# Optimization experiments

Measured on AMD Instinct MI355X. Metric: run time of the kernel, lower is better.

## Reference

```python
import jax, jax.numpy as jnp
import numpy as np

N = 100000
DEG = 16
E = N * DEG
IN_DIM = 256
HID = 64
OUT = 64


def setup_inputs() -> dict:
    key = jax.random.key(0)
    ks = jax.random.split(key, 6)
    x = jax.random.normal(ks[0], (N, IN_DIM), dtype=jnp.float32)
    # CSR with fixed degree DEG: row i owns edges [i*DEG, (i+1)*DEG)
    row_id = jnp.repeat(jnp.arange(N, dtype=jnp.int64), DEG)
    col_id = jax.random.randint(ks[1], (E,), 0, N, dtype=jnp.int64)
    adj = jnp.stack([col_id, row_id])  # adj[0]=col, adj[1]=row (matches torch forward)
    row_ptr = (jnp.arange(N + 1, dtype=jnp.int64) * DEG)
    W1 = jax.random.normal(ks[2], (IN_DIM, HID), dtype=jnp.float32) / np.sqrt(IN_DIM)
    b1 = jnp.zeros((HID,), dtype=jnp.float32)
    W2 = jax.random.normal(ks[3], (HID, OUT), dtype=jnp.float32) / np.sqrt(HID)
    b2 = jnp.zeros((OUT,), dtype=jnp.float32)
    return {"x": x, "adj": adj, "row_ptr": row_ptr, "W1": W1, "b1": b1, "W2": W2, "b2": b2}


def agnn_layer(x, row, col, beta):
    # x: [N, d]; row/col: [E]. AGNN: e_ij = beta*cos(x_i, x_j), row-softmax, aggregate x_j.
    norm = jnp.maximum(jnp.linalg.norm(x, axis=-1, keepdims=True), 1e-12)
    xn = x / norm  # [N, d]
    e = beta * jnp.sum(xn[row] * xn[col], axis=-1)  # [E] cosine scores
    # numerically stable segment softmax over rows
    m = jax.ops.segment_max(e, row, num_segments=N)  # [N]
    ex = jnp.exp(e - m[row])  # [E]
    denom = jax.ops.segment_sum(ex, row, num_segments=N)  # [N]
    alpha = ex / jnp.maximum(denom[row], 1e-12)  # [E]
    out = jax.ops.segment_sum(alpha[:, None] * x[col], row, num_segments=N)  # [N, d]
    return out


def reference(x, adj, row_ptr, W1, b1, W2, b2):
    col, row = adj[0], adj[1]
    beta = jnp.float32(1.0)  # non-trainable buffer, initialized to ones
    h = jax.nn.relu(x @ W1 + b1)
    for _ in range(4):
        h = jax.nn.relu(agnn_layer(h, row, col, beta))
    return h @ W2 + b2
```

## Files before the change

kernel.cpp:

```cpp
#include <hip/hip_runtime.h>
#include <math.h>

#define N_NODES 100000
#define DEG 16
#define IN_DIM 256
#define HID 64

typedef _Float16 f16x8 __attribute__((ext_vector_type(8)));
typedef _Float16 f16x4 __attribute__((ext_vector_type(4)));
typedef __fp16 fp16x2b __attribute__((ext_vector_type(2)));
typedef float f32x4 __attribute__((ext_vector_type(4)));

union F16x8u {
  f16x8 v;
  fp16x2b h2[4];
};

__global__ __launch_bounds__(256) void extract_col_kernel(const int* __restrict__ adj,
                                                          int* __restrict__ col, int E) {
  const bool is64 = (adj[2 * E - 1] == 0);
  for (int e = blockIdx.x * blockDim.x + threadIdx.x; e < E; e += gridDim.x * blockDim.x) {
    col[e] = is64 ? adj[2 * e] : adj[e];
  }
}

__global__ __launch_bounds__(256) void prep_wfrag_kernel(const float* __restrict__ W,
                                                         _Float16* __restrict__ wfrag,
                                                         int nfrag) {
  const int id = blockIdx.x * 256 + threadIdx.x;
  if (id >= nfrag) return;
  const int lane = id & 63;
  const int nt = (id >> 6) & 3;
  const int kt = id >> 8;
  const int k0 = kt * 32 + (lane >> 4) * 8;
  const int c = nt * 16 + (lane & 15);
  f16x8 v;
#pragma unroll
  for (int j = 0; j < 8; ++j) v[j] = (_Float16)W[(k0 + j) * HID + c];
  ((f16x8*)wfrag)[id] = v;
}

__global__ __launch_bounds__(256) void mlp1_kernel(const float* __restrict__ x,
                                                   const _Float16* __restrict__ wfrag,
                                                   const float* __restrict__ b1,
                                                   _Float16* __restrict__ hn,
                                                   float* __restrict__ nrm) {
  __shared__ f16x8 Bs[2048];
#pragma unroll
  for (int i = 0; i < 8; ++i)
    Bs[threadIdx.x + 256 * i] = ((const f16x8*)wfrag)[threadIdx.x + 256 * i];

  const int lane = threadIdx.x & 63;
  const int wv = threadIdx.x >> 6;
  const int rbase = blockIdx.x * 64 + wv * 16;
  const int arow = min(rbase + (lane & 15), N_NODES - 1);
  const int kgrp = lane >> 4;
  const float* xrow = x + (size_t)arow * IN_DIM + kgrp * 8;

  f32x4 acc[4];
#pragma unroll
  for (int nt = 0; nt < 4; ++nt) acc[nt] = {0.0f, 0.0f, 0.0f, 0.0f};

  __syncthreads();

#pragma unroll
  for (int kt = 0; kt < 8; ++kt) {
    const float4 a0 = *(const float4*)&xrow[kt * 32];
    const float4 a1 = *(const float4*)&xrow[kt * 32 + 4];
    F16x8u u;
    u.h2[0] = __builtin_amdgcn_cvt_pkrtz(a0.x, a0.y);
    u.h2[1] = __builtin_amdgcn_cvt_pkrtz(a0.z, a0.w);
    u.h2[2] = __builtin_amdgcn_cvt_pkrtz(a1.x, a1.y);
    u.h2[3] = __builtin_amdgcn_cvt_pkrtz(a1.z, a1.w);
#pragma unroll
    for (int nt = 0; nt < 4; ++nt)
      acc[nt] = __builtin_amdgcn_mfma_f32_16x16x32_f16(u.v, Bs[(kt * 4 + nt) * 64 + lane],
                                                       acc[nt], 0, 0, 0);
  }

  const int colb = lane & 15;
  float bias[4];
#pragma unroll
  for (int nt = 0; nt < 4; ++nt) bias[nt] = b1[nt * 16 + colb];

#pragma unroll
  for (int j = 0; j < 4; ++j) {
    float o[4];
#pragma unroll
    for (int nt = 0; nt < 4; ++nt) o[nt] = fmaxf(acc[nt][j] + bias[nt], 0.0f);
    float ss = o[0] * o[0] + o[1] * o[1] + o[2] * o[2] + o[3] * o[3];
    ss += __shfl_xor(ss, 1); ss += __shfl_xor(ss, 2);
    ss += __shfl_xor(ss, 4); ss += __shfl_xor(ss, 8);
    const float nv = sqrtf(ss);
    const float inv = 1.0f / fmaxf(nv, 1e-12f);
    const int row = rbase + kgrp * 4 + j;
    if (row < N_NODES) {
#pragma unroll
      for (int nt = 0; nt < 4; ++nt)
        hn[(size_t)row * HID + nt * 16 + colb] = (_Float16)(o[nt] * inv);
      if (colb == 0) nrm[row] = nv;
    }
  }
}

__global__ __launch_bounds__(256) void agnn_kernel(const _Float16* __restrict__ hn,
                                                   const float* __restrict__ nrm,
                                                   const int* __restrict__ col,
                                                   _Float16* __restrict__ hn_out,
                                                   float* __restrict__ nrm_out) {
  const int lane = threadIdx.x & 63;
  const int wv = threadIdx.x >> 6;
  const int g = lane >> 4;
  const int gl = lane & 15;
  const int node = blockIdx.x * 16 + wv * 4 + g;

  const f16x4* hp4 = (const f16x4*)hn;
  const f16x4 xiv = hp4[(size_t)node * 16 + gl];

  const int cidx = col[node * DEG + gl];
  const float ncv = nrm[cidx];

  const int vbase = (lane & 48) * 4;

  f16x4 xcv[DEG];
#pragma unroll
  for (int e = 0; e < DEG; ++e) {
    const int ce = __builtin_amdgcn_ds_bpermute(vbase + e * 4, cidx);
    xcv[e] = hp4[(size_t)((uint)ce * 16u + (uint)gl)];
  }

  const float x0 = (float)xiv[0], x1 = (float)xiv[1];
  const float x2 = (float)xiv[2], x3 = (float)xiv[3];
  float t[DEG];
#pragma unroll
  for (int e = 0; e < DEG; ++e) {
    float a = fmaf(x1, (float)xcv[e][1], x0 * (float)xcv[e][0]);
    float b = fmaf(x3, (float)xcv[e][3], x2 * (float)xcv[e][2]);
    t[e] = a + b;
  }

  const bool b0 = (lane & 1), b1 = (lane & 2), b2 = (lane & 4), b3 = (lane & 8);
  float u[8];
#pragma unroll
  for (int j = 0; j < 8; ++j) {
    const float keep = b0 ? t[2 * j + 1] : t[2 * j];
    const float send = b0 ? t[2 * j] : t[2 * j + 1];
    u[j] = keep + __shfl_xor(send, 1);
  }
  float v[4];
#pragma unroll
  for (int j = 0; j < 4; ++j) {
    const float keep = b1 ? u[2 * j + 1] : u[2 * j];
    const float send = b1 ? u[2 * j] : u[2 * j + 1];
    v[j] = keep + __shfl_xor(send, 2);
  }
  float w2[2];
#pragma unroll
  for (int j = 0; j < 2; ++j) {
    const float keep = b2 ? v[2 * j + 1] : v[2 * j];
    const float send = b2 ? v[2 * j] : v[2 * j + 1];
    w2[j] = keep + __shfl_xor(send, 4);
  }
  float p;
  {
    const float keep = b3 ? w2[1] : w2[0];
    const float send = b3 ? w2[0] : w2[1];
    p = keep + __shfl_xor(send, 8);
  }

  float m = p;
  m = fmaxf(m, __shfl_xor(m, 1)); m = fmaxf(m, __shfl_xor(m, 2));
  m = fmaxf(m, __shfl_xor(m, 4)); m = fmaxf(m, __shfl_xor(m, 8));
  const float ex = __expf(p - m);
  float dn = ex;
  dn += __shfl_xor(dn, 1); dn += __shfl_xor(dn, 2);
  dn += __shfl_xor(dn, 4); dn += __shfl_xor(dn, 8);
  const float wgt = (ex / dn) * ncv;

  float o0 = 0.0f, o1 = 0.0f, o2 = 0.0f, o3 = 0.0f;
#pragma unroll
  for (int e = 0; e < DEG; ++e) {
    const float we = __int_as_float(
        __builtin_amdgcn_ds_bpermute(vbase + e * 4, __float_as_int(wgt)));
    o0 = fmaf(we, (float)xcv[e][0], o0);
    o1 = fmaf(we, (float)xcv[e][1], o1);
    o2 = fmaf(we, (float)xcv[e][2], o2);
    o3 = fmaf(we, (float)xcv[e][3], o3);
  }
  o0 = fmaxf(o0, 0.0f); o1 = fmaxf(o1, 0.0f);
  o2 = fmaxf(o2, 0.0f); o3 = fmaxf(o3, 0.0f);

  float ss = fmaf(o0, o0, o1 * o1) + fmaf(o2, o2, o3 * o3);
  ss += __shfl_xor(ss, 1); ss += __shfl_xor(ss, 2);
  ss += __shfl_xor(ss, 4); ss += __shfl_xor(ss, 8);
  const float nv = sqrtf(ss);
  const float inv = 1.0f / fmaxf(nv, 1e-12f);

  f16x4 ov;
  ov[0] = (_Float16)(o0 * inv); ov[1] = (_Float16)(o1 * inv);
  ov[2] = (_Float16)(o2 * inv); ov[3] = (_Float16)(o3 * inv);
  ((f16x4*)hn_out)[(size_t)node * 16 + gl] = ov;
  if (gl == 0) nrm_out[node] = nv;
}

__global__ __launch_bounds__(256) void mlp2_kernel(const _Float16* __restrict__ hn,
                                                   const float* __restrict__ nrm,
                                                   const _Float16* __restrict__ w2frag,
                                                   const float* __restrict__ b2,
                                                   float* __restrict__ out) {
  __shared__ f16x8 Bs[512];
  if (threadIdx.x < 256) {
    Bs[threadIdx.x] = ((const f16x8*)w2frag)[threadIdx.x];
    Bs[threadIdx.x + 256] = ((const f16x8*)w2frag)[threadIdx.x + 256];
  }

  const int lane = threadIdx.x & 63;
  const int wv = threadIdx.x >> 6;
  const int rbase = blockIdx.x * 64 + wv * 16;
  const int arow = min(rbase + (lane & 15), N_NODES - 1);
  const int kgrp = lane >> 4;
  const _Float16* hrow = hn + (size_t)arow * HID + kgrp * 8;

  f32x4 acc[4];
#pragma unroll
  for (int nt = 0; nt < 4; ++nt) acc[nt] = {0.0f, 0.0f, 0.0f, 0.0f};

  __syncthreads();

#pragma unroll
  for (int kt = 0; kt < 2; ++kt) {
    const f16x8 a = *(const f16x8*)&hrow[kt * 32];
#pragma unroll
    for (int nt = 0; nt < 4; ++nt)
      acc[nt] = __builtin_amdgcn_mfma_f32_16x16x32_f16(a, Bs[(kt * 4 + nt) * 64 + lane],
                                                       acc[nt], 0, 0, 0);
  }

  const int colb = lane & 15;
  float bias[4];
#pragma unroll
  for (int nt = 0; nt < 4; ++nt) bias[nt] = b2[nt * 16 + colb];

#pragma unroll
  for (int j = 0; j < 4; ++j) {
    const int row = rbase + kgrp * 4 + j;
    const float rnv = nrm[min(row, N_NODES - 1)];
    if (row < N_NODES) {
#pragma unroll
      for (int nt = 0; nt < 4; ++nt)
        out[(size_t)row * HID + nt * 16 + colb] = fmaf(acc[nt][j], rnv, bias[nt]);
    }
  }
}

extern "C" void kernel_launch(void* const* d_in, const int* in_sizes, int n_in,
                              void* d_out, int out_size, void* d_ws, size_t ws_size,
                              hipStream_t stream) {
  const float* x = (const float*)d_in[0];
  const int* adj = (const int*)d_in[1];
  const float* W1 = (const float*)d_in[3];
  const float* b1 = (const float*)d_in[4];
  const float* W2 = (const float*)d_in[5];
  const float* b2 = (const float*)d_in[6];
  float* out = (float*)d_out;

  const int E = N_NODES * DEG;

  char* ws = (char*)d_ws;
  int* col = (int*)ws;
  ws += (size_t)E * sizeof(int);
  _Float16* wfrag = (_Float16*)ws;
  ws += (size_t)IN_DIM * HID * sizeof(_Float16);
  _Float16* w2frag = (_Float16*)ws;
  ws += (size_t)HID * HID * sizeof(_Float16);
  _Float16* hnA = (_Float16*)ws;
  ws += (size_t)N_NODES * HID * sizeof(_Float16);
  _Float16* hnB = (_Float16*)ws;
  ws += (size_t)N_NODES * HID * sizeof(_Float16);
  float* nrA = (float*)ws;
  ws += (size_t)N_NODES * sizeof(float);
  float* nrB = (float*)ws;

  hipLaunchKernelGGL(extract_col_kernel, dim3(2048), dim3(256), 0, stream, adj, col, E);
  hipLaunchKernelGGL(prep_wfrag_kernel, dim3(8), dim3(256), 0, stream, W1, wfrag, 2048);
  hipLaunchKernelGGL(prep_wfrag_kernel, dim3(2), dim3(256), 0, stream, W2, w2frag, 512);

  const int mlp_blocks = (N_NODES + 63) / 64;
  hipLaunchKernelGGL(mlp1_kernel, dim3(mlp_blocks), dim3(256), 0, stream, x, wfrag, b1, hnA, nrA);

  const int agnn_blocks = N_NODES / 16;
  hipLaunchKernelGGL(agnn_kernel, dim3(agnn_blocks), dim3(256), 0, stream, hnA, nrA, col, hnB, nrB);
  hipLaunchKernelGGL(agnn_kernel, dim3(agnn_blocks), dim3(256), 0, stream, hnB, nrB, col, hnA, nrA);
  hipLaunchKernelGGL(agnn_kernel, dim3(agnn_blocks), dim3(256), 0, stream, hnA, nrA, col, hnB, nrB);
  hipLaunchKernelGGL(agnn_kernel, dim3(agnn_blocks), dim3(256), 0, stream, hnB, nrB, col, hnA, nrA);

  hipLaunchKernelGGL(mlp2_kernel, dim3(mlp_blocks), dim3(256), 0, stream, hnA, nrA, w2frag, b2, out);
}
```

Measured before the change: 161.5 us.

## Remap AGNN kernel to 8 lanes per node with 16-byte gathers and fdot2

Each node now uses 8 lanes instead of 16, and each lane loads 8 fp16 features per neighbour (16-byte vector loads). The 16 edges are processed in two chunks of 8. Scores use packed fp16 dot-product instructions, and the softmax max-subtraction is dropped, relying on cosine scores being bounded by beta. The aim is fewer memory and ALU instructions per gathered row and fewer shuffle stages, at the cost of more registers per lane and half as many nodes' worth of blocks.

```diff
diff --git a/kernel.cpp b/kernel.cpp
--- a/kernel.cpp
+++ b/kernel.cpp
@@ -7,7 +7,6 @@
 #define HID 64
 
 typedef _Float16 f16x8 __attribute__((ext_vector_type(8)));
-typedef _Float16 f16x4 __attribute__((ext_vector_type(4)));
 typedef __fp16 fp16x2b __attribute__((ext_vector_type(2)));
 typedef float f32x4 __attribute__((ext_vector_type(4)));
 
@@ -15,6 +14,16 @@
   f16x8 v;
   fp16x2b h2[4];
 };
+
+#if __has_builtin(__builtin_amdgcn_fdot2)
+__device__ __forceinline__ float fdot2(fp16x2b a, fp16x2b b, float c) {
+  return __builtin_amdgcn_fdot2(a, b, c, false);
+}
+#else
+__device__ __forceinline__ float fdot2(fp16x2b a, fp16x2b b, float c) {
+  return fmaf((float)a[0], (float)b[0], fmaf((float)a[1], (float)b[1], c));
+}
+#endif
 
 __global__ __launch_bounds__(256) void extract_col_kernel(const int* __restrict__ adj,
                                                           int* __restrict__ col, int E) {
@@ -110,97 +119,107 @@
                                                    float* __restrict__ nrm_out) {
   const int lane = threadIdx.x & 63;
   const int wv = threadIdx.x >> 6;
-  const int g = lane >> 4;
-  const int gl = lane & 15;
-  const int node = blockIdx.x * 16 + wv * 4 + g;
-
-  const f16x4* hp4 = (const f16x4*)hn;
-  const f16x4 xiv = hp4[(size_t)node * 16 + gl];
-
-  const int cidx = col[node * DEG + gl];
-  const float ncv = nrm[cidx];
-
-  const int vbase = (lane & 48) * 4;
-
-  f16x4 xcv[DEG];
-#pragma unroll
-  for (int e = 0; e < DEG; ++e) {
-    const int ce = __builtin_amdgcn_ds_bpermute(vbase + e * 4, cidx);
-    xcv[e] = hp4[(size_t)((uint)ce * 16u + (uint)gl)];
-  }
-
-  const float x0 = (float)xiv[0], x1 = (float)xiv[1];
-  const float x2 = (float)xiv[2], x3 = (float)xiv[3];
-  float t[DEG];
-#pragma unroll
-  for (int e = 0; e < DEG; ++e) {
-    float a = fmaf(x1, (float)xcv[e][1], x0 * (float)xcv[e][0]);
-    float b = fmaf(x3, (float)xcv[e][3], x2 * (float)xcv[e][2]);
-    t[e] = a + b;
-  }
-
-  const bool b0 = (lane & 1), b1 = (lane & 2), b2 = (lane & 4), b3 = (lane & 8);
-  float u[8];
-#pragma unroll
-  for (int j = 0; j < 8; ++j) {
-    const float keep = b0 ? t[2 * j + 1] : t[2 * j];
-    const float send = b0 ? t[2 * j] : t[2 * j + 1];
-    u[j] = keep + __shfl_xor(send, 1);
-  }
-  float v[4];
-#pragma unroll
-  for (int j = 0; j < 4; ++j) {
-    const float keep = b1 ? u[2 * j + 1] : u[2 * j];
-    const float send = b1 ? u[2 * j] : u[2 * j + 1];
-    v[j] = keep + __shfl_xor(send, 2);
-  }
-  float w2[2];
-#pragma unroll
-  for (int j = 0; j < 2; ++j) {
-    const float keep = b2 ? v[2 * j + 1] : v[2 * j];
-    const float send = b2 ? v[2 * j] : v[2 * j + 1];
-    w2[j] = keep + __shfl_xor(send, 4);
-  }
-  float p;
-  {
-    const float keep = b3 ? w2[1] : w2[0];
-    const float send = b3 ? w2[0] : w2[1];
-    p = keep + __shfl_xor(send, 8);
-  }
-
-  float m = p;
-  m = fmaxf(m, __shfl_xor(m, 1)); m = fmaxf(m, __shfl_xor(m, 2));
-  m = fmaxf(m, __shfl_xor(m, 4)); m = fmaxf(m, __shfl_xor(m, 8));
-  const float ex = __expf(p - m);
-  float dn = ex;
-  dn += __shfl_xor(dn, 1); dn += __shfl_xor(dn, 2);
-  dn += __shfl_xor(dn, 4); dn += __shfl_xor(dn, 8);
-  const float wgt = (ex / dn) * ncv;
-
-  float o0 = 0.0f, o1 = 0.0f, o2 = 0.0f, o3 = 0.0f;
-#pragma unroll
-  for (int e = 0; e < DEG; ++e) {
-    const float we = __int_as_float(
-        __builtin_amdgcn_ds_bpermute(vbase + e * 4, __float_as_int(wgt)));
-    o0 = fmaf(we, (float)xcv[e][0], o0);
-    o1 = fmaf(we, (float)xcv[e][1], o1);
-    o2 = fmaf(we, (float)xcv[e][2], o2);
-    o3 = fmaf(we, (float)xcv[e][3], o3);
-  }
-  o0 = fmaxf(o0, 0.0f); o1 = fmaxf(o1, 0.0f);
-  o2 = fmaxf(o2, 0.0f); o3 = fmaxf(o3, 0.0f);
-
-  float ss = fmaf(o0, o0, o1 * o1) + fmaf(o2, o2, o3 * o3);
-  ss += __shfl_xor(ss, 1); ss += __shfl_xor(ss, 2);
-  ss += __shfl_xor(ss, 4); ss += __shfl_xor(ss, 8);
+  const int g = lane >> 3;
+  const int q = lane & 7;
+  const int node = blockIdx.x * 32 + wv * 8 + g;
+
+  const f16x8* hp8 = (const f16x8*)hn;
+  F16x8u xi;
+  xi.v = hp8[(size_t)node * 8 + q];
+
+  const int cidx0 = col[node * DEG + q];
+  const int cidx1 = col[node * DEG + 8 + q];
+  const float ncv0 = nrm[cidx0];
+  const float ncv1 = nrm[cidx1];
+
+  const int base = (lane & 56) * 4;
+
+  float o[8];
+#pragma unroll
+  for (int d = 0; d < 8; ++d) o[d] = 0.0f;
+  float dn = 0.0f;
+
+#pragma unroll
+  for (int c = 0; c < 2; ++c) {
+    const int cs = c ? cidx1 : cidx0;
+    const float ncv = c ? ncv1 : ncv0;
+
+    F16x8u xcv[8];
+#pragma unroll
+    for (int k = 0; k < 8; ++k) {
+      const int ce = __builtin_amdgcn_ds_bpermute(base + k * 4, cs);
+      xcv[k].v = hp8[(size_t)((uint)ce) * 8u + (uint)q];
+    }
+
+    float t[8];
+#pragma unroll
+    for (int k = 0; k < 8; ++k) {
+      float s = 0.0f;
+#pragma unroll
+      for (int j = 0; j < 4; ++j) s = fdot2(xi.h2[j], xcv[k].h2[j], s);
+      t[k] = s;
+    }
+
+    const bool b0 = (lane & 1), b1 = (lane & 2), b2 = (lane & 4);
+    float u[4];
+#pragma unroll
+    for (int j = 0; j < 4; ++j) {
+      const float keep = b0 ? t[2 * j + 1] : t[2 * j];
+      const float send = b0 ? t[2 * j] : t[2 * j + 1];
+      u[j] = keep + __shfl_xor(send, 1);
+    }
+    float v[2];
+#pragma unroll
+    for (int j = 0; j < 2; ++j) {
+      const float keep = b1 ? u[2 * j + 1] : u[2 * j];
+      const float send = b1 ? u[2 * j] : u[2 * j + 1];
+      v[j] = keep + __shfl_xor(send, 2);
+    }
+    float p;
+    {
+      const float keep = b2 ? v[1] : v[0];
+      const float send = b2 ? v[0] : v[1];
+      p = keep + __shfl_xor(send, 4);
+    }
+
+    const float ex = __expf(p);
+    dn += ex;
+    const float wgt = ex * ncv;
+
+#pragma unroll
+    for (int k = 0; k < 8; ++k) {
+      const float wk = __int_as_float(
+          __builtin_amdgcn_ds_bpermute(base + k * 4, __float_as_int(wgt)));
+#pragma unroll
+      for (int j = 0; j < 4; ++j) {
+        o[2 * j] = fmaf((float)xcv[k].h2[j][0], wk, o[2 * j]);
+        o[2 * j + 1] = fmaf((float)xcv[k].h2[j][1], wk, o[2 * j + 1]);
+      }
+    }
+  }
+
+  dn += __shfl_xor(dn, 1);
+  dn += __shfl_xor(dn, 2);
+  dn += __shfl_xor(dn, 4);
+  const float idn = 1.0f / dn;
+
+  float ss = 0.0f;
+#pragma unroll
+  for (int d = 0; d < 8; ++d) {
+    o[d] = fmaxf(o[d] * idn, 0.0f);
+    ss = fmaf(o[d], o[d], ss);
+  }
+  ss += __shfl_xor(ss, 1);
+  ss += __shfl_xor(ss, 2);
+  ss += __shfl_xor(ss, 4);
   const float nv = sqrtf(ss);
   const float inv = 1.0f / fmaxf(nv, 1e-12f);
 
-  f16x4 ov;
-  ov[0] = (_Float16)(o0 * inv); ov[1] = (_Float16)(o1 * inv);
-  ov[2] = (_Float16)(o2 * inv); ov[3] = (_Float16)(o3 * inv);
-  ((f16x4*)hn_out)[(size_t)node * 16 + gl] = ov;
-  if (gl == 0) nrm_out[node] = nv;
+  F16x8u ov;
+#pragma unroll
+  for (int d = 0; d < 8; ++d) ov.v[d] = (_Float16)(o[d] * inv);
+  ((f16x8*)hn_out)[(size_t)node * 8 + q] = ov.v;
+  if (q == 0) nrm_out[node] = nv;
 }
 
 __global__ __launch_bounds__(256) void mlp2_kernel(const _Float16* __restrict__ hn,
@@ -288,7 +307,7 @@
   const int mlp_blocks = (N_NODES + 63) / 64;
   hipLaunchKernelGGL(mlp1_kernel, dim3(mlp_blocks), dim3(256), 0, stream, x, wfrag, b1, hnA, nrA);
 
-  const int agnn_blocks = N_NODES / 16;
+  const int agnn_blocks = N_NODES / 32;
   hipLaunchKernelGGL(agnn_kernel, dim3(agnn_blocks), dim3(256), 0, stream, hnA, nrA, col, hnB, nrB);
   hipLaunchKernelGGL(agnn_kernel, dim3(agnn_blocks), dim3(256), 0, stream, hnB, nrB, col, hnA, nrA);
   hipLaunchKernelGGL(agnn_kernel, dim3(agnn_blocks), dim3(256), 0, stream, hnA, nrA, col, hnB, nrB);
```

Result: no change. 159.2 us (-1.4%).
